# Performance work log

Measured on AMD Instinct MI355X. Metric: run time of the kernel, lower is better.

Reference implementation:

```python
import jax, jax.numpy as jnp
import numpy as np

D_MODEL = 1024
N_HEADS = 16
HEAD_DIM = D_MODEL // N_HEADS


def setup_inputs() -> dict:
    key = jax.random.key(0)
    ks = jax.random.split(key, 5)
    x = jax.random.normal(ks[0], (4, 2048, D_MODEL), dtype=jnp.float32)
    # Linear params (torch Linear: y = x @ W.T + b); store W as [in, out] for einsum.
    s_in = 1.0 / np.sqrt(D_MODEL)
    w_in = jax.random.uniform(ks[1], (D_MODEL, 3 * D_MODEL), jnp.float32, -s_in, s_in)
    b_in = jax.random.uniform(ks[2], (3 * D_MODEL,), jnp.float32, -s_in, s_in)
    w_out = jax.random.uniform(ks[3], (D_MODEL, D_MODEL), jnp.float32, -s_in, s_in)
    b_out = jax.random.uniform(ks[4], (D_MODEL,), jnp.float32, -s_in, s_in)
    return {"x": x, "w_in": w_in, "b_in": b_in, "w_out": w_out, "b_out": b_out}


def reference(x, w_in, b_in, w_out, b_out):
    B, L, D = x.shape
    H, Hd = N_HEADS, HEAD_DIM
    qkv = jnp.einsum('bld,de->ble', x, w_in) + b_in  # [B,L,3D]
    q, k, v = jnp.split(qkv, 3, axis=-1)
    # [B,H,L,Hd]
    q = q.reshape(B, L, H, Hd).transpose(0, 2, 1, 3)
    k = k.reshape(B, L, H, Hd).transpose(0, 2, 1, 3)
    v = v.reshape(B, L, H, Hd).transpose(0, 2, 1, 3)
    scale = 1.0 / np.sqrt(Hd).astype(np.float32)
    scores = jnp.einsum('bhqd,bhkd->bhqk', q, k) * scale  # [B,H,L,L]
    causal = jnp.tril(jnp.ones((L, L), dtype=bool))
    scores = jnp.where(causal, scores, jnp.finfo(scores.dtype).min)
    attn = jax.nn.softmax(scores, axis=-1)
    out = jnp.einsum('bhqk,bhkd->bhqd', attn, v)  # [B,H,L,Hd]
    out = out.transpose(0, 2, 1, 3).reshape(B, L, D)
    return jnp.einsum('bld,de->ble', out, w_out) + b_out
```

## Files before the change

kernel.cpp:

```cpp
#include <hip/hip_runtime.h>

typedef float f32x4 __attribute__((ext_vector_type(4)));
typedef __bf16 bf16x8 __attribute__((ext_vector_type(8)));
typedef short s16x8 __attribute__((ext_vector_type(8)));
typedef int i32x4 __attribute__((ext_vector_type(4)));

__device__ __forceinline__ unsigned short f2bf(float f) {
  union { float f; unsigned u; } v;
  v.f = f;
  unsigned r = v.u + 0x7FFFu + ((v.u >> 16) & 1u);
  return (unsigned short)(r >> 16);
}

__device__ __forceinline__ int cvt_pk_bf16(float lo, float hi) {
  int d;
  asm("v_cvt_pk_bf16_f32 %0, %1, %2" : "=v"(d) : "v"(lo), "v"(hi));
  return d;
}

__device__ __forceinline__ float max3f(float a, float b, float c) {
  float d;
  asm("v_max3_f32 %0, %1, %2, %3" : "=v"(d) : "v"(a), "v"(b), "v"(c));
  return d;
}

#if __has_builtin(__builtin_amdgcn_exp2f)
__device__ __forceinline__ float fexp2(float x) { return __builtin_amdgcn_exp2f(x); }
#else
__device__ __forceinline__ float fexp2(float x) { return exp2f(x); }
#endif

__device__ __forceinline__ void gl_lds16(const void* g, void* l) {
  __builtin_amdgcn_global_load_lds(
      (__attribute__((address_space(1))) void*)g,
      (__attribute__((address_space(3))) void*)l, 16, 0, 0);
}

__device__ __forceinline__ void transpose_cvt_body(const float* __restrict__ in,
                                                   short* __restrict__ out,
                                                   int R, int C, int bx, int by, int tid) {
  __shared__ short tile[32][33];
  int c0 = bx * 32, r0 = by * 32;
  int tx = tid & 31, ty = tid >> 5;
#pragma unroll
  for (int i = 0; i < 32; i += 8)
    tile[ty + i][tx] = (short)f2bf(in[(size_t)(r0 + ty + i) * C + c0 + tx]);
  __syncthreads();
#pragma unroll
  for (int i = 0; i < 32; i += 8)
    out[(size_t)(c0 + ty + i) * R + r0 + tx] = tile[tx][ty + i];
}

__global__ __launch_bounds__(256) void k_prep(const float* __restrict__ x,
                                              short* __restrict__ x_bf,
                                              const float* __restrict__ w_in,
                                              short* __restrict__ w_inT,
                                              const float* __restrict__ w_out,
                                              short* __restrict__ w_outT) {
  const int bid = blockIdx.x;
  const int tid = threadIdx.x;
  if (bid < 4096) {
    int i = (bid * 256 + tid) * 8;
    const float4* p = (const float4*)(x + i);
    float4 a = p[0], b = p[1];
    s16x8 r;
    r[0] = (short)f2bf(a.x); r[1] = (short)f2bf(a.y);
    r[2] = (short)f2bf(a.z); r[3] = (short)f2bf(a.w);
    r[4] = (short)f2bf(b.x); r[5] = (short)f2bf(b.y);
    r[6] = (short)f2bf(b.z); r[7] = (short)f2bf(b.w);
    *(s16x8*)(x_bf + i) = r;
  } else if (bid < 4096 + 3072) {
    const int local = bid - 4096;
    transpose_cvt_body(w_in, w_inT, 1024, 3072, local % 96, local / 96, tid);
  } else {
    const int local = bid - (4096 + 3072);
    transpose_cvt_body(w_out, w_outT, 1024, 1024, local % 32, local / 32, tid);
  }
}

__global__ __launch_bounds__(256) void k_qkv_gemm(const short* __restrict__ A,
                                                  const short* __restrict__ B,
                                                  const float* __restrict__ bias,
                                                  short* __restrict__ qb,
                                                  short* __restrict__ kb,
                                                  short* __restrict__ vtb) {
  __shared__ short As[128 * 64];
  __shared__ short Bs[128 * 64];
  const int tid = threadIdx.x;
  const int lane = tid & 63;
  const int w = tid >> 6;
  const int g = lane >> 4, c = lane & 15;
  const int orig = blockIdx.y * 24 + blockIdx.x;
  const int wgs = (orig & 7) * 192 + (orig >> 3);
  const int m0 = (wgs / 24) * 128, n0 = (wgs % 24) * 128;
  const int wm = (w >> 1) * 64, wn = (w & 1) * 64;
  f32x4 acc[4][4] = {};

  const int srow = tid >> 3, schunk = tid & 7;
  const int sgx = schunk ^ (srow & 7);
  const short* aP = A + (size_t)(m0 + srow) * 1024 + sgx * 8;
  const short* bP = B + (size_t)(n0 + srow) * 1024 + sgx * 8;
  short* lA = As + srow * 64 + schunk * 8;
  short* lB = Bs + srow * 64 + schunk * 8;

  for (int k0 = 0; k0 < 1024; k0 += 64) {
#pragma unroll
    for (int t = 0; t < 4; t++) {
      gl_lds16(aP + (size_t)(t * 32) * 1024 + k0, lA + t * 32 * 64);
      gl_lds16(bP + (size_t)(t * 32) * 1024 + k0, lB + t * 32 * 64);
    }
    __syncthreads();
#pragma unroll
    for (int kd = 0; kd < 2; kd++) {
      bf16x8 af[4], bfr[4];
#pragma unroll
      for (int t = 0; t < 4; t++) {
        int ra = wm + t * 16 + c;
        af[t] = *(const bf16x8*)(As + ra * 64 + ((kd * 4 + g) ^ (ra & 7)) * 8);
        int rb = wn + t * 16 + c;
        bfr[t] = *(const bf16x8*)(Bs + rb * 64 + ((kd * 4 + g) ^ (rb & 7)) * 8);
      }
#pragma unroll
      for (int i = 0; i < 4; i++)
#pragma unroll
        for (int jn = 0; jn < 4; jn++)
          acc[i][jn] = __builtin_amdgcn_mfma_f32_16x16x32_bf16(af[i], bfr[jn], acc[i][jn], 0, 0, 0);
    }
    __syncthreads();
  }

  const int which = n0 >> 10;
  const float qscale = 0.125f * 1.4426950408889634f;
  if (which == 2) {
#pragma unroll
    for (int jn = 0; jn < 4; jn++) {
      const int col = n0 + wn + jn * 16 + c;
      const float bv = bias[col];
      const int cw = col & 1023;
      const int h = cw >> 6, d = cw & 63;
#pragma unroll
      for (int i = 0; i < 4; i++) {
        const int row = m0 + wm + i * 16 + g * 4;
        const int bb = row >> 11, l0 = row & 2047;
        int lo = cvt_pk_bf16(acc[i][jn][0] + bv, acc[i][jn][1] + bv);
        int hi = cvt_pk_bf16(acc[i][jn][2] + bv, acc[i][jn][3] + bv);
        *(int2*)(vtb + (size_t)((bb * 16 + h) * 64 + d) * 2048 + l0) = make_int2(lo, hi);
      }
    }
  } else {
    short* dst = (which == 0) ? qb : kb;
    const float sc = (which == 0) ? qscale : 1.0f;
#pragma unroll
    for (int jn = 0; jn < 4; jn++) {
      const int col = n0 + wn + jn * 16 + c;
      const float bv = bias[col];
      const int cw = col & 1023;
      const int h = cw >> 6, d = cw & 63;
#pragma unroll
      for (int i = 0; i < 4; i++) {
#pragma unroll
        for (int r = 0; r < 4; r++) {
          const int row = m0 + wm + i * 16 + g * 4 + r;
          const int bb = row >> 11, l = row & 2047;
          dst[((size_t)((bb * 16 + h) * 2048 + l) << 6) + d] = (short)f2bf((acc[i][jn][r] + bv) * sc);
        }
      }
    }
  }
}

__device__ __forceinline__ int sigma_row(int rho) {
  return ((rho >> 5) << 5) | (((rho >> 2) & 3) << 3) | (((rho >> 4) & 1) << 2) | (rho & 3);
}

__device__ __forceinline__ void stage_kv512(const short* __restrict__ Kt,
                                            const short* __restrict__ Vtt,
                                            short* ksb, short* vsb, int tid) {
#pragma unroll
  for (int t = 0; t < 2; t++) {
    int p = tid + t * 512;
    int krow = p >> 3, kchk = (p & 7) ^ (krow & 7);
    gl_lds16(Kt + (size_t)sigma_row(krow) * 64 + kchk * 8, ksb + p * 8);
    int dv = p >> 4, vchk = (p & 15) ^ (dv & 15);
    gl_lds16(Vtt + (size_t)dv * 2048 + vchk * 8, vsb + p * 8);
  }
}

__global__ __launch_bounds__(512, 2) void k_attn(const short* __restrict__ Q,
                                                 const short* __restrict__ K,
                                                 const short* __restrict__ Vt,
                                                 short* __restrict__ O) {
  __shared__ short Ks[2][128 * 64];
  __shared__ short Vs[2][64 * 128];
  const int tid = threadIdx.x;
  const int lane = tid & 63;
  const int w = tid >> 6;
  const int quad = lane >> 4, cq = lane & 15;
  const int bh = blockIdx.y;
  const int bb = bh >> 4, h = bh & 15;
  const size_t base = (size_t)bh * (2048 * 64);
  const int pr = blockIdx.x;
  const int qhi = 15 - pr, qlo = pr;
  const int jmax = qhi;
  const int qloc = w * 16 + cq;

  bf16x8 qf[2][2];
#pragma unroll
  for (int mt = 0; mt < 2; mt++) {
    const int qt = mt ? qlo : qhi;
#pragma unroll
    for (int kd = 0; kd < 2; kd++)
      qf[mt][kd] = *(const bf16x8*)(Q + base +
          (size_t)(qt * 128 + w * 16 + cq) * 64 + (kd * 4 + quad) * 8);
  }

  stage_kv512(K + base, Vt + base, Ks[0], Vs[0], tid);

  f32x4 o[2][4] = {};
  float m_run[2] = {-1e30f, -1e30f};
  float l_run[2] = {0.f, 0.f};

  for (int j = 0; j <= jmax; j++) {
    const int cur = j & 1;
    __syncthreads();
    if (j < jmax)
      stage_kv512(K + base + (size_t)(j + 1) * 128 * 64, Vt + base + (j + 1) * 128,
                  Ks[cur ^ 1], Vs[cur ^ 1], tid);
    const short* ks = Ks[cur];
    const short* vs = Vs[cur];
    const bool act1 = (j <= qlo);

    f32x4 s[2][8] = {};
    __builtin_amdgcn_s_setprio(1);
    if (act1) {
#pragma unroll
      for (int kd = 0; kd < 2; kd++)
#pragma unroll
        for (int nt = 0; nt < 8; nt++) {
          int krow = nt * 16 + cq;
          bf16x8 kf = *(const bf16x8*)(ks + krow * 64 + ((kd * 4 + quad) ^ (krow & 7)) * 8);
          s[0][nt] = __builtin_amdgcn_mfma_f32_16x16x32_bf16(kf, qf[0][kd], s[0][nt], 0, 0, 0);
          s[1][nt] = __builtin_amdgcn_mfma_f32_16x16x32_bf16(kf, qf[1][kd], s[1][nt], 0, 0, 0);
        }
    } else {
#pragma unroll
      for (int kd = 0; kd < 2; kd++)
#pragma unroll
        for (int nt = 0; nt < 8; nt++) {
          int krow = nt * 16 + cq;
          bf16x8 kf = *(const bf16x8*)(ks + krow * 64 + ((kd * 4 + quad) ^ (krow & 7)) * 8);
          s[0][nt] = __builtin_amdgcn_mfma_f32_16x16x32_bf16(kf, qf[0][kd], s[0][nt], 0, 0, 0);
        }
    }
    __builtin_amdgcn_s_setprio(0);

    bf16x8 pf[2][4];
    const int nmt = act1 ? 2 : 1;
#pragma unroll
    for (int mt = 0; mt < 2; mt++) {
      if (mt >= nmt) break;
      const bool diag = (j == (mt ? qlo : qhi));
      if (diag) {
#pragma unroll
        for (int nt = 0; nt < 8; nt++)
#pragma unroll
          for (int r = 0; r < 4; r++) {
            int key = (nt >> 1) * 32 + (nt & 1) * 4 + r;
            if (key + quad * 8 > qloc) s[mt][nt][r] = -1e30f;
          }
      }
      float mx;
      {
        float pm[8];
#pragma unroll
        for (int nt = 0; nt < 8; nt++)
          pm[nt] = fmaxf(max3f(s[mt][nt][0], s[mt][nt][1], s[mt][nt][2]), s[mt][nt][3]);
        mx = max3f(max3f(pm[0], pm[1], pm[2]), max3f(pm[3], pm[4], pm[5]),
                   fmaxf(pm[6], pm[7]));
      }
      mx = fmaxf(mx, __shfl_xor(mx, 16));
      mx = fmaxf(mx, __shfl_xor(mx, 32));

      float mn = m_run[mt];
      if (!__all(mx - mn <= 8.0f)) {
        const float nm = fmaxf(mn, mx);
        const float alpha = fexp2(mn - nm);
        m_run[mt] = nm;
        l_run[mt] *= alpha;
#pragma unroll
        for (int dn = 0; dn < 4; dn++) o[mt][dn] *= alpha;
        mn = nm;
      }

      float lt = 0.f;
#pragma unroll
      for (int nt = 0; nt < 8; nt++)
#pragma unroll
        for (int r = 0; r < 4; r++) {
          float p = fexp2(s[mt][nt][r] - mn);
          s[mt][nt][r] = p;
          lt += p;
        }
      l_run[mt] += lt;
#pragma unroll
      for (int kt = 0; kt < 4; kt++) {
        i32x4 ow;
        ow[0] = cvt_pk_bf16(s[mt][2 * kt][0], s[mt][2 * kt][1]);
        ow[1] = cvt_pk_bf16(s[mt][2 * kt][2], s[mt][2 * kt][3]);
        ow[2] = cvt_pk_bf16(s[mt][2 * kt + 1][0], s[mt][2 * kt + 1][1]);
        ow[3] = cvt_pk_bf16(s[mt][2 * kt + 1][2], s[mt][2 * kt + 1][3]);
        pf[mt][kt] = __builtin_bit_cast(bf16x8, ow);
      }
    }

    __builtin_amdgcn_s_setprio(1);
    if (act1) {
#pragma unroll
      for (int kt = 0; kt < 4; kt++)
#pragma unroll
        for (int dn = 0; dn < 4; dn++) {
          int drow = dn * 16 + cq;
          bf16x8 vtf = *(const bf16x8*)(vs + drow * 128 + ((kt * 4 + quad) ^ (drow & 15)) * 8);
          o[0][dn] = __builtin_amdgcn_mfma_f32_16x16x32_bf16(vtf, pf[0][kt], o[0][dn], 0, 0, 0);
          o[1][dn] = __builtin_amdgcn_mfma_f32_16x16x32_bf16(vtf, pf[1][kt], o[1][dn], 0, 0, 0);
        }
    } else {
#pragma unroll
      for (int kt = 0; kt < 4; kt++)
#pragma unroll
        for (int dn = 0; dn < 4; dn++) {
          int drow = dn * 16 + cq;
          bf16x8 vtf = *(const bf16x8*)(vs + drow * 128 + ((kt * 4 + quad) ^ (drow & 15)) * 8);
          o[0][dn] = __builtin_amdgcn_mfma_f32_16x16x32_bf16(vtf, pf[0][kt], o[0][dn], 0, 0, 0);
        }
    }
    __builtin_amdgcn_s_setprio(0);
  }

#pragma unroll
  for (int mt = 0; mt < 2; mt++) {
    const int qt = mt ? qlo : qhi;
    float lf = l_run[mt];
    lf += __shfl_xor(lf, 16);
    lf += __shfl_xor(lf, 32);
    const float inv = 1.f / lf;
    const size_t rb = ((size_t)(bb * 2048 + qt * 128 + w * 16 + cq)) * 1024 + h * 64;
#pragma unroll
    for (int dn = 0; dn < 4; dn++) {
      int d0 = cvt_pk_bf16(o[mt][dn][0] * inv, o[mt][dn][1] * inv);
      int d1 = cvt_pk_bf16(o[mt][dn][2] * inv, o[mt][dn][3] * inv);
      *(int2*)(O + rb + dn * 16 + quad * 4) = make_int2(d0, d1);
    }
  }
}

__global__ __launch_bounds__(256) void k_out_gemm(const short* __restrict__ A,
                                                  const short* __restrict__ B,
                                                  const float* __restrict__ bias,
                                                  float* __restrict__ out) {
  __shared__ short As[128 * 64];
  __shared__ short Bs[128 * 64];
  const int tid = threadIdx.x;
  const int lane = tid & 63;
  const int w = tid >> 6;
  const int g = lane >> 4, c = lane & 15;
  const int orig = blockIdx.y * 8 + blockIdx.x;
  const int wgs = (orig & 7) * 64 + (orig >> 3);
  const int m0 = (wgs >> 3) * 128, n0 = (wgs & 7) * 128;
  const int wm = (w >> 1) * 64, wn = (w & 1) * 64;
  f32x4 acc[4][4] = {};

  const int srow = tid >> 3, schunk = tid & 7;
  const int sgx = schunk ^ (srow & 7);
  const short* aP = A + (size_t)(m0 + srow) * 1024 + sgx * 8;
  const short* bP = B + (size_t)(n0 + srow) * 1024 + sgx * 8;
  short* lA = As + srow * 64 + schunk * 8;
  short* lB = Bs + srow * 64 + schunk * 8;

  for (int k0 = 0; k0 < 1024; k0 += 64) {
#pragma unroll
    for (int t = 0; t < 4; t++) {
      gl_lds16(aP + (size_t)(t * 32) * 1024 + k0, lA + t * 32 * 64);
      gl_lds16(bP + (size_t)(t * 32) * 1024 + k0, lB + t * 32 * 64);
    }
    __syncthreads();
#pragma unroll
    for (int kd = 0; kd < 2; kd++) {
      bf16x8 af[4], bfr[4];
#pragma unroll
      for (int t = 0; t < 4; t++) {
        int ra = wm + t * 16 + c;
        af[t] = *(const bf16x8*)(As + ra * 64 + ((kd * 4 + g) ^ (ra & 7)) * 8);
        int rb = wn + t * 16 + c;
        bfr[t] = *(const bf16x8*)(Bs + rb * 64 + ((kd * 4 + g) ^ (rb & 7)) * 8);
      }
#pragma unroll
      for (int i = 0; i < 4; i++)
#pragma unroll
        for (int jn = 0; jn < 4; jn++)
          acc[i][jn] = __builtin_amdgcn_mfma_f32_16x16x32_bf16(af[i], bfr[jn], acc[i][jn], 0, 0, 0);
    }
    __syncthreads();
  }
#pragma unroll
  for (int jn = 0; jn < 4; jn++) {
    const int col = n0 + wn + jn * 16 + c;
    const float bv = bias[col];
#pragma unroll
    for (int i = 0; i < 4; i++) {
#pragma unroll
      for (int r = 0; r < 4; r++) {
        const int row = m0 + wm + i * 16 + g * 4 + r;
        out[(size_t)row * 1024 + col] = acc[i][jn][r] + bv;
      }
    }
  }
}

extern "C" void kernel_launch(void* const* d_in, const int* in_sizes, int n_in,
                              void* d_out, int out_size, void* d_ws, size_t ws_size,
                              hipStream_t stream) {
  const float* x     = (const float*)d_in[0];
  const float* w_in  = (const float*)d_in[1];
  const float* b_in  = (const float*)d_in[2];
  const float* w_out = (const float*)d_in[3];
  const float* b_out = (const float*)d_in[4];
  float* out = (float*)d_out;
  char* ws = (char*)d_ws;
  short* x_bf   = (short*)(ws);
  short* w_inT  = (short*)(ws + (16ull << 20));
  short* w_outT = (short*)(ws + (22ull << 20));
  short* qb     = (short*)(ws + (24ull << 20));
  short* kb     = (short*)(ws + (40ull << 20));
  short* vtb    = (short*)(ws + (56ull << 20));
  short* ao     = (short*)(ws + (72ull << 20));

  k_prep<<<dim3(8192), dim3(256), 0, stream>>>(x, x_bf, w_in, w_inT, w_out, w_outT);
  k_qkv_gemm<<<dim3(24, 64), dim3(256), 0, stream>>>(x_bf, w_inT, b_in, qb, kb, vtb);
  k_attn<<<dim3(8, 64), dim3(512), 0, stream>>>(qb, kb, vtb, ao);
  k_out_gemm<<<dim3(8, 64), dim3(256), 0, stream>>>(ao, w_outT, b_out, out);
}
```

Measured before the change: 256.4 us.

## Pair query tiles as pr and pr+8 and interleave dual-tile softmax

Changes the query-tile pairing from (15-pr, pr) to (8+pr, pr). The softmax for both tiles is now written as interleaved straight-line code with split partial sums, and the conditional lazy rescale is replaced by an unconditional one. The interleaving exposes more independent exp and convert work for latency hiding. The new pairing changes how causal work is spread across blocks and could unbalance them, and the rescale multiplies now run on every iteration.

```diff
diff --git a/kernel.cpp b/kernel.cpp
--- a/kernel.cpp
+++ b/kernel.cpp
@@ -200,7 +200,7 @@
   const int bb = bh >> 4, h = bh & 15;
   const size_t base = (size_t)bh * (2048 * 64);
   const int pr = blockIdx.x;
-  const int qhi = 15 - pr, qlo = pr;
+  const int qhi = 8 + pr, qlo = pr;
   const int jmax = qhi;
   const int qloc = w * 16 + cq;
 
@@ -255,62 +255,98 @@
     __builtin_amdgcn_s_setprio(0);
 
     bf16x8 pf[2][4];
-    const int nmt = act1 ? 2 : 1;
-#pragma unroll
-    for (int mt = 0; mt < 2; mt++) {
-      if (mt >= nmt) break;
-      const bool diag = (j == (mt ? qlo : qhi));
-      if (diag) {
+    if (act1) {
+      if (j == qlo) {
 #pragma unroll
         for (int nt = 0; nt < 8; nt++)
 #pragma unroll
           for (int r = 0; r < 4; r++) {
             int key = (nt >> 1) * 32 + (nt & 1) * 4 + r;
-            if (key + quad * 8 > qloc) s[mt][nt][r] = -1e30f;
+            if (key + quad * 8 > qloc) s[1][nt][r] = -1e30f;
           }
       }
-      float mx;
-      {
-        float pm[8];
+      float pm0[8], pm1[8];
+#pragma unroll
+      for (int nt = 0; nt < 8; nt++) {
+        pm0[nt] = fmaxf(max3f(s[0][nt][0], s[0][nt][1], s[0][nt][2]), s[0][nt][3]);
+        pm1[nt] = fmaxf(max3f(s[1][nt][0], s[1][nt][1], s[1][nt][2]), s[1][nt][3]);
+      }
+      float mx0 = max3f(max3f(pm0[0], pm0[1], pm0[2]), max3f(pm0[3], pm0[4], pm0[5]),
+                        fmaxf(pm0[6], pm0[7]));
+      float mx1 = max3f(max3f(pm1[0], pm1[1], pm1[2]), max3f(pm1[3], pm1[4], pm1[5]),
+                        fmaxf(pm1[6], pm1[7]));
+      mx0 = fmaxf(mx0, __shfl_xor(mx0, 16));
+      mx1 = fmaxf(mx1, __shfl_xor(mx1, 16));
+      mx0 = fmaxf(mx0, __shfl_xor(mx0, 32));
+      mx1 = fmaxf(mx1, __shfl_xor(mx1, 32));
+      const float mn0 = fmaxf(m_run[0], mx0), mn1 = fmaxf(m_run[1], mx1);
+      const float al0 = fexp2(m_run[0] - mn0), al1 = fexp2(m_run[1] - mn1);
+      m_run[0] = mn0; m_run[1] = mn1;
+      float lt0a = 0.f, lt0b = 0.f, lt1a = 0.f, lt1b = 0.f;
+#pragma unroll
+      for (int kt = 0; kt < 4; kt++) {
+        float a0 = fexp2(s[0][2 * kt][0] - mn0), a1 = fexp2(s[0][2 * kt][1] - mn0);
+        float a2 = fexp2(s[0][2 * kt][2] - mn0), a3 = fexp2(s[0][2 * kt][3] - mn0);
+        float b0 = fexp2(s[0][2 * kt + 1][0] - mn0), b1 = fexp2(s[0][2 * kt + 1][1] - mn0);
+        float b2 = fexp2(s[0][2 * kt + 1][2] - mn0), b3 = fexp2(s[0][2 * kt + 1][3] - mn0);
+        float c0 = fexp2(s[1][2 * kt][0] - mn1), c1 = fexp2(s[1][2 * kt][1] - mn1);
+        float c2 = fexp2(s[1][2 * kt][2] - mn1), c3 = fexp2(s[1][2 * kt][3] - mn1);
+        float d0 = fexp2(s[1][2 * kt + 1][0] - mn1), d1 = fexp2(s[1][2 * kt + 1][1] - mn1);
+        float d2 = fexp2(s[1][2 * kt + 1][2] - mn1), d3 = fexp2(s[1][2 * kt + 1][3] - mn1);
+        lt0a += (a0 + a1) + (a2 + a3);
+        lt0b += (b0 + b1) + (b2 + b3);
+        lt1a += (c0 + c1) + (c2 + c3);
+        lt1b += (d0 + d1) + (d2 + d3);
+        i32x4 ow0, ow1;
+        ow0[0] = cvt_pk_bf16(a0, a1); ow0[1] = cvt_pk_bf16(a2, a3);
+        ow0[2] = cvt_pk_bf16(b0, b1); ow0[3] = cvt_pk_bf16(b2, b3);
+        ow1[0] = cvt_pk_bf16(c0, c1); ow1[1] = cvt_pk_bf16(c2, c3);
+        ow1[2] = cvt_pk_bf16(d0, d1); ow1[3] = cvt_pk_bf16(d2, d3);
+        pf[0][kt] = __builtin_bit_cast(bf16x8, ow0);
+        pf[1][kt] = __builtin_bit_cast(bf16x8, ow1);
+      }
+      l_run[0] = l_run[0] * al0 + (lt0a + lt0b);
+      l_run[1] = l_run[1] * al1 + (lt1a + lt1b);
+#pragma unroll
+      for (int dn = 0; dn < 4; dn++) { o[0][dn] *= al0; o[1][dn] *= al1; }
+    } else {
+      if (j == jmax) {
 #pragma unroll
         for (int nt = 0; nt < 8; nt++)
-          pm[nt] = fmaxf(max3f(s[mt][nt][0], s[mt][nt][1], s[mt][nt][2]), s[mt][nt][3]);
-        mx = max3f(max3f(pm[0], pm[1], pm[2]), max3f(pm[3], pm[4], pm[5]),
-                   fmaxf(pm[6], pm[7]));
-      }
-      mx = fmaxf(mx, __shfl_xor(mx, 16));
-      mx = fmaxf(mx, __shfl_xor(mx, 32));
-
-      float mn = m_run[mt];
-      if (!__all(mx - mn <= 8.0f)) {
-        const float nm = fmaxf(mn, mx);
-        const float alpha = fexp2(mn - nm);
-        m_run[mt] = nm;
-        l_run[mt] *= alpha;
-#pragma unroll
-        for (int dn = 0; dn < 4; dn++) o[mt][dn] *= alpha;
-        mn = nm;
-      }
-
-      float lt = 0.f;
+#pragma unroll
+          for (int r = 0; r < 4; r++) {
+            int key = (nt >> 1) * 32 + (nt & 1) * 4 + r;
+            if (key + quad * 8 > qloc) s[0][nt][r] = -1e30f;
+          }
+      }
+      float pm0[8];
 #pragma unroll
       for (int nt = 0; nt < 8; nt++)
-#pragma unroll
-        for (int r = 0; r < 4; r++) {
-          float p = fexp2(s[mt][nt][r] - mn);
-          s[mt][nt][r] = p;
-          lt += p;
-        }
-      l_run[mt] += lt;
+        pm0[nt] = fmaxf(max3f(s[0][nt][0], s[0][nt][1], s[0][nt][2]), s[0][nt][3]);
+      float mx0 = max3f(max3f(pm0[0], pm0[1], pm0[2]), max3f(pm0[3], pm0[4], pm0[5]),
+                        fmaxf(pm0[6], pm0[7]));
+      mx0 = fmaxf(mx0, __shfl_xor(mx0, 16));
+      mx0 = fmaxf(mx0, __shfl_xor(mx0, 32));
+      const float mn0 = fmaxf(m_run[0], mx0);
+      const float al0 = fexp2(m_run[0] - mn0);
+      m_run[0] = mn0;
+      float lt0a = 0.f, lt0b = 0.f;
 #pragma unroll
       for (int kt = 0; kt < 4; kt++) {
-        i32x4 ow;
-        ow[0] = cvt_pk_bf16(s[mt][2 * kt][0], s[mt][2 * kt][1]);
-        ow[1] = cvt_pk_bf16(s[mt][2 * kt][2], s[mt][2 * kt][3]);
-        ow[2] = cvt_pk_bf16(s[mt][2 * kt + 1][0], s[mt][2 * kt + 1][1]);
-        ow[3] = cvt_pk_bf16(s[mt][2 * kt + 1][2], s[mt][2 * kt + 1][3]);
-        pf[mt][kt] = __builtin_bit_cast(bf16x8, ow);
-      }
+        float a0 = fexp2(s[0][2 * kt][0] - mn0), a1 = fexp2(s[0][2 * kt][1] - mn0);
+        float a2 = fexp2(s[0][2 * kt][2] - mn0), a3 = fexp2(s[0][2 * kt][3] - mn0);
+        float b0 = fexp2(s[0][2 * kt + 1][0] - mn0), b1 = fexp2(s[0][2 * kt + 1][1] - mn0);
+        float b2 = fexp2(s[0][2 * kt + 1][2] - mn0), b3 = fexp2(s[0][2 * kt + 1][3] - mn0);
+        lt0a += (a0 + a1) + (a2 + a3);
+        lt0b += (b0 + b1) + (b2 + b3);
+        i32x4 ow0;
+        ow0[0] = cvt_pk_bf16(a0, a1); ow0[1] = cvt_pk_bf16(a2, a3);
+        ow0[2] = cvt_pk_bf16(b0, b1); ow0[3] = cvt_pk_bf16(b2, b3);
+        pf[0][kt] = __builtin_bit_cast(bf16x8, ow0);
+      }
+      l_run[0] = l_run[0] * al0 + (lt0a + lt0b);
+#pragma unroll
+      for (int dn = 0; dn < 4; dn++) o[0][dn] *= al0;
     }
 
     __builtin_amdgcn_s_setprio(1);
```

After: 265.3 us. 1.03x slower.

## Rewrite QKV GEMM as 256x256 double-buffered pipelined kernel with 8 waves

Applied to the files above, without the earlier changes.

The QKV projection GEMM moves from 128x128 tiles with 4 waves and a single LDS buffer to 256x256 tiles with 8 waves and double-buffered LDS. Global-to-LDS staging of the next K tile is interleaved with MFMA phases, using explicit barriers, vmcnt waits and s_setprio to overlap memory and compute. This removes the load/sync stall of each K step and raises data reuse per tile. The cost is more registers (8x4 accumulators), more LDS (128 KB), and only 384 blocks, which may leave CUs underfilled.

```diff
diff --git a/kernel.cpp b/kernel.cpp
--- a/kernel.cpp
+++ b/kernel.cpp
@@ -78,91 +78,141 @@
   }
 }
 
-__global__ __launch_bounds__(256) void k_qkv_gemm(const short* __restrict__ A,
-                                                  const short* __restrict__ B,
-                                                  const float* __restrict__ bias,
-                                                  short* __restrict__ qb,
-                                                  short* __restrict__ kb,
-                                                  short* __restrict__ vtb) {
-  __shared__ short As[128 * 64];
-  __shared__ short Bs[128 * 64];
+
+#define STG(SRC, DST, BUF, HALF, KT)                                          \
+  {                                                                           \
+    _Pragma("unroll")                                                         \
+    for (int q_ = 0; q_ < 2; q_++)                                            \
+      gl_lds16(SRC + (size_t)((HALF)*128 + q_ * 64) * 1024 + (KT)*64,         \
+               DST[BUF] + ((HALF)*128 + q_ * 64) * 64 + ldst);                \
+  }
+
+#define QPH(BUF, MH, KD, BREAD, VM, ...)                                      \
+  {                                                                           \
+    const short* as_ = SA[BUF];                                               \
+    bf16x8 af_[4];                                                            \
+    _Pragma("unroll")                                                         \
+    for (int m_ = 0; m_ < 4; m_++)                                            \
+      af_[m_] = *(const bf16x8*)(as_ + aoff + ((MH)*4 + m_) * 1024 +          \
+                                 ((KD) ? xk1 : xk0));                         \
+    if (BREAD) {                                                              \
+      const short* bs_ = SB[BUF];                                             \
+      _Pragma("unroll")                                                       \
+      for (int n_ = 0; n_ < 4; n_++)                                          \
+        bfr[n_] = *(const bf16x8*)(bs_ + boff + n_ * 1024 +                   \
+                                   ((KD) ? xk1 : xk0));                       \
+    }                                                                         \
+    __VA_ARGS__;                                                              \
+    __builtin_amdgcn_s_barrier();                                             \
+    asm volatile("s_waitcnt lgkmcnt(0)" ::: "memory");                        \
+    __builtin_amdgcn_s_setprio(1);                                            \
+    _Pragma("unroll")                                                         \
+    for (int m_ = 0; m_ < 4; m_++)                                            \
+      _Pragma("unroll")                                                       \
+      for (int n_ = 0; n_ < 4; n_++)                                          \
+        acc[(MH)*4 + m_][n_] = __builtin_amdgcn_mfma_f32_16x16x32_bf16(       \
+            af_[m_], bfr[n_], acc[(MH)*4 + m_][n_], 0, 0, 0);                 \
+    __builtin_amdgcn_s_setprio(0);                                            \
+    if ((VM) == 2) asm volatile("s_waitcnt vmcnt(2)" ::: "memory");           \
+    if ((VM) == 0) asm volatile("s_waitcnt vmcnt(0)" ::: "memory");           \
+    __builtin_amdgcn_s_barrier();                                             \
+  }
+
+__global__ __launch_bounds__(512, 2) void k_qkv_gemm(const short* __restrict__ A,
+                                                     const short* __restrict__ B,
+                                                     const float* __restrict__ bias,
+                                                     short* __restrict__ qb,
+                                                     short* __restrict__ kb,
+                                                     short* __restrict__ vtb) {
+  __shared__ short SA[2][256 * 64];
+  __shared__ short SB[2][256 * 64];
   const int tid = threadIdx.x;
   const int lane = tid & 63;
+  const int quad = lane >> 4, cq = lane & 15;
   const int w = tid >> 6;
-  const int g = lane >> 4, c = lane & 15;
-  const int orig = blockIdx.y * 24 + blockIdx.x;
-  const int wgs = (orig & 7) * 192 + (orig >> 3);
-  const int m0 = (wgs / 24) * 128, n0 = (wgs % 24) * 128;
-  const int wm = (w >> 1) * 64, wn = (w & 1) * 64;
-  f32x4 acc[4][4] = {};
+  const int wmi = w >> 2, wni = w & 3;
+
+  const int orig = blockIdx.y * 12 + blockIdx.x;
+  const int wg = (orig & 7) * 48 + (orig >> 3);
+  const int bn = wg % 12, bm = wg / 12;
+  const int m0 = bm * 256, n0 = bn * 256;
 
   const int srow = tid >> 3, schunk = tid & 7;
   const int sgx = schunk ^ (srow & 7);
-  const short* aP = A + (size_t)(m0 + srow) * 1024 + sgx * 8;
-  const short* bP = B + (size_t)(n0 + srow) * 1024 + sgx * 8;
-  short* lA = As + srow * 64 + schunk * 8;
-  short* lB = Bs + srow * 64 + schunk * 8;
-
-  for (int k0 = 0; k0 < 1024; k0 += 64) {
-#pragma unroll
-    for (int t = 0; t < 4; t++) {
-      gl_lds16(aP + (size_t)(t * 32) * 1024 + k0, lA + t * 32 * 64);
-      gl_lds16(bP + (size_t)(t * 32) * 1024 + k0, lB + t * 32 * 64);
-    }
-    __syncthreads();
-#pragma unroll
-    for (int kd = 0; kd < 2; kd++) {
-      bf16x8 af[4], bfr[4];
-#pragma unroll
-      for (int t = 0; t < 4; t++) {
-        int ra = wm + t * 16 + c;
-        af[t] = *(const bf16x8*)(As + ra * 64 + ((kd * 4 + g) ^ (ra & 7)) * 8);
-        int rb = wn + t * 16 + c;
-        bfr[t] = *(const bf16x8*)(Bs + rb * 64 + ((kd * 4 + g) ^ (rb & 7)) * 8);
-      }
-#pragma unroll
-      for (int i = 0; i < 4; i++)
-#pragma unroll
-        for (int jn = 0; jn < 4; jn++)
-          acc[i][jn] = __builtin_amdgcn_mfma_f32_16x16x32_bf16(af[i], bfr[jn], acc[i][jn], 0, 0, 0);
-    }
-    __syncthreads();
-  }
+  const short* aSrc = A + (size_t)(m0 + srow) * 1024 + sgx * 8;
+  const short* bSrc = B + (size_t)(n0 + srow) * 1024 + sgx * 8;
+  const int ldst = srow * 64 + schunk * 8;
+
+  const int aoff = (wmi * 128 + cq) * 64;
+  const int boff = (wni * 64 + cq) * 64;
+  const int xk0 = (quad ^ (cq & 7)) * 8;
+  const int xk1 = ((4 + quad) ^ (cq & 7)) * 8;
+
+  f32x4 acc[8][4] = {};
+  bf16x8 bfr[4];
+
+  STG(aSrc, SA, 0, 0, 0);
+  STG(aSrc, SA, 0, 1, 0);
+  STG(bSrc, SB, 0, 0, 0);
+  STG(bSrc, SB, 0, 1, 0);
+  STG(aSrc, SA, 1, 0, 1);
+  asm volatile("s_waitcnt vmcnt(2)" ::: "memory");
+  __builtin_amdgcn_s_barrier();
+
+  for (int i = 0; i < 7; ++i) {
+    const int T = 2 * i;
+    QPH(0, 0, 0, 1, -1, STG(aSrc, SA, 1, 1, T + 1));
+    QPH(0, 1, 0, 0, -1, STG(bSrc, SB, 1, 0, T + 1));
+    QPH(0, 0, 1, 1, -1, STG(bSrc, SB, 1, 1, T + 1));
+    QPH(0, 1, 1, 0,  2, STG(aSrc, SA, 0, 0, T + 2));
+    QPH(1, 0, 0, 1, -1, STG(aSrc, SA, 0, 1, T + 2));
+    QPH(1, 1, 0, 0, -1, STG(bSrc, SB, 0, 0, T + 2));
+    QPH(1, 0, 1, 1, -1, STG(bSrc, SB, 0, 1, T + 2));
+    QPH(1, 1, 1, 0,  2, STG(aSrc, SA, 1, 0, T + 3));
+  }
+  QPH(0, 0, 0, 1, -1, STG(aSrc, SA, 1, 1, 15));
+  QPH(0, 1, 0, 0, -1, STG(bSrc, SB, 1, 0, 15));
+  QPH(0, 0, 1, 1, -1, STG(bSrc, SB, 1, 1, 15));
+  QPH(0, 1, 1, 0,  0, (void)0);
+  QPH(1, 0, 0, 1, -1, (void)0);
+  QPH(1, 1, 0, 0, -1, (void)0);
+  QPH(1, 0, 1, 1, -1, (void)0);
+  QPH(1, 1, 1, 0, -1, (void)0);
 
   const int which = n0 >> 10;
   const float qscale = 0.125f * 1.4426950408889634f;
   if (which == 2) {
 #pragma unroll
-    for (int jn = 0; jn < 4; jn++) {
-      const int col = n0 + wn + jn * 16 + c;
+    for (int fn = 0; fn < 4; fn++) {
+      const int col = n0 + wni * 64 + fn * 16 + cq;
       const float bv = bias[col];
       const int cw = col & 1023;
       const int h = cw >> 6, d = cw & 63;
 #pragma unroll
-      for (int i = 0; i < 4; i++) {
-        const int row = m0 + wm + i * 16 + g * 4;
-        const int bb = row >> 11, l0 = row & 2047;
-        int lo = cvt_pk_bf16(acc[i][jn][0] + bv, acc[i][jn][1] + bv);
-        int hi = cvt_pk_bf16(acc[i][jn][2] + bv, acc[i][jn][3] + bv);
-        *(int2*)(vtb + (size_t)((bb * 16 + h) * 64 + d) * 2048 + l0) = make_int2(lo, hi);
+      for (int fm = 0; fm < 8; fm++) {
+        const int row = m0 + wmi * 128 + fm * 16 + quad * 4;
+        const int bb2 = row >> 11, l0 = row & 2047;
+        int lo = cvt_pk_bf16(acc[fm][fn][0] + bv, acc[fm][fn][1] + bv);
+        int hi = cvt_pk_bf16(acc[fm][fn][2] + bv, acc[fm][fn][3] + bv);
+        *(int2*)(vtb + (size_t)((bb2 * 16 + h) * 64 + d) * 2048 + l0) = make_int2(lo, hi);
       }
     }
   } else {
     short* dst = (which == 0) ? qb : kb;
     const float sc = (which == 0) ? qscale : 1.0f;
 #pragma unroll
-    for (int jn = 0; jn < 4; jn++) {
-      const int col = n0 + wn + jn * 16 + c;
+    for (int fn = 0; fn < 4; fn++) {
+      const int col = n0 + wni * 64 + fn * 16 + cq;
       const float bv = bias[col];
       const int cw = col & 1023;
       const int h = cw >> 6, d = cw & 63;
 #pragma unroll
-      for (int i = 0; i < 4; i++) {
+      for (int fm = 0; fm < 8; fm++) {
 #pragma unroll
         for (int r = 0; r < 4; r++) {
-          const int row = m0 + wm + i * 16 + g * 4 + r;
-          const int bb = row >> 11, l = row & 2047;
-          dst[((size_t)((bb * 16 + h) * 2048 + l) << 6) + d] = (short)f2bf((acc[i][jn][r] + bv) * sc);
+          const int row = m0 + wmi * 128 + fm * 16 + quad * 4 + r;
+          const int bb2 = row >> 11, l = row & 2047;
+          dst[((size_t)((bb2 * 16 + h) * 2048 + l) << 6) + d] = (short)f2bf((acc[fm][fn][r] + bv) * sc);
         }
       }
     }
@@ -436,7 +486,7 @@
   short* ao     = (short*)(ws + (72ull << 20));
 
   k_prep<<<dim3(8192), dim3(256), 0, stream>>>(x, x_bf, w_in, w_inT, w_out, w_outT);
-  k_qkv_gemm<<<dim3(24, 64), dim3(256), 0, stream>>>(x_bf, w_inT, b_in, qb, kb, vtb);
+  k_qkv_gemm<<<dim3(12, 32), dim3(512), 0, stream>>>(x_bf, w_inT, b_in, qb, kb, vtb);
   k_attn<<<dim3(8, 64), dim3(512), 0, stream>>>(qb, kb, vtb, ao);
   k_out_gemm<<<dim3(8, 64), dim3(256), 0, stream>>>(ao, w_outT, b_out, out);
 }
```

Measured after the change: 264.6 us. 1.03x slower.
